# Kernel optimization log

Hardware: AMD Instinct MI355X
Metric: run time of the kernel (lower is better)

The kernel has to match this reference:

```python
import jax, jax.numpy as jnp
import numpy as np

B, L, E = 16, 1022, 1280
D, H, FF, NL = 512, 8, 2048, 4
DH = D // H
EPS = 1e-5


def layer_norm(x, s, b):
    m = jnp.mean(x, axis=-1, keepdims=True)
    v = jnp.mean(jnp.square(x - m), axis=-1, keepdims=True)
    return (x - m) * jax.lax.rsqrt(v + EPS) * s + b


def setup_inputs() -> dict:
    key = jax.random.key(0)
    ks = jax.random.split(key, 12)
    s = 0.02
    return {
        "embeddings": jax.random.normal(ks[0], (B, L, E), jnp.float32),
        "mask": jnp.ones((B, L), jnp.float32),
        "position": jnp.tile(jnp.arange(L, dtype=jnp.int32)[None, :], (B, 1)),
        "proj_w": jax.random.normal(ks[1], (D, E), jnp.float32) * s,
        "proj_b": jnp.zeros((D,), jnp.float32),
        "proj_ln_s": jnp.ones((D,), jnp.float32),
        "proj_ln_b": jnp.zeros((D,), jnp.float32),
        "ln1_s": jnp.ones((NL, D), jnp.float32),
        "ln1_b": jnp.zeros((NL, D), jnp.float32),
        "in_w": jax.random.normal(ks[2], (NL, 3 * D, D), jnp.float32) * s,
        "in_b": jnp.zeros((NL, 3 * D), jnp.float32),
        "out_w": jax.random.normal(ks[3], (NL, D, D), jnp.float32) * s,
        "out_b": jnp.zeros((NL, D), jnp.float32),
        "ln2_s": jnp.ones((NL, D), jnp.float32),
        "ln2_b": jnp.zeros((NL, D), jnp.float32),
        "w1": jax.random.normal(ks[4], (NL, FF, D), jnp.float32) * s,
        "b1": jnp.zeros((NL, FF), jnp.float32),
        "w2": jax.random.normal(ks[5], (NL, D, FF), jnp.float32) * s,
        "b2": jnp.zeros((NL, D), jnp.float32),
        "h1_w": jax.random.normal(ks[6], (128, 2 * D), jnp.float32) * s,
        "h1_b": jnp.zeros((128,), jnp.float32),
        "hln_s": jnp.ones((128,), jnp.float32),
        "hln_b": jnp.zeros((128,), jnp.float32),
        "h2_w": jax.random.normal(ks[7], (1, 128), jnp.float32) * s,
        "h2_b": jnp.zeros((1,), jnp.float32),
    }


def _rope_tables():
    inv_freq = 1.0 / (10000.0 ** (jnp.arange(0, DH, 2, dtype=jnp.float32) / DH))
    t = jnp.arange(L, dtype=jnp.float32)
    freqs = jnp.outer(t, inv_freq)          # [L, DH/2]
    emb = jnp.concatenate([freqs, freqs], axis=-1)  # [L, DH]
    return jnp.cos(emb), jnp.sin(emb)


def _rotate_half(x):
    x1, x2 = jnp.split(x, 2, axis=-1)
    return jnp.concatenate([-x2, x1], axis=-1)


def _apply_rope(x, cos, sin):
    # x: [B, L, D] -> per-head rotation -> [B, L, D]
    xh = x.reshape(B, L, H, DH)
    xh = xh * cos[None, :, None, :] + _rotate_half(xh) * sin[None, :, None, :]
    return xh.reshape(B, L, D)


def _forward(embeddings, mask, proj_w, proj_b, proj_ln_s, proj_ln_b,
             ln1_s, ln1_b, in_w, in_b, out_w, out_b, ln2_s, ln2_b,
             w1, b1, w2, b2, h1_w, h1_b, hln_s, hln_b, h2_w, h2_b):
    cos, sin = _rope_tables()
    x = layer_norm(embeddings @ proj_w.T + proj_b, proj_ln_s, proj_ln_b)  # [B,L,D]
    pad = mask <= 0  # True where padded (~mask.bool())
    scale = 1.0 / jnp.sqrt(jnp.float32(DH))
    for i in range(NL):
        n = layer_norm(x, ln1_s[i], ln1_b[i])
        q_in = _apply_rope(n, cos, sin)
        k_in = _apply_rope(n, cos, sin)
        v_in = n
        wq, wk, wv = jnp.split(in_w[i], 3, axis=0)
        bq, bk, bv = jnp.split(in_b[i], 3, axis=0)
        qh = (q_in @ wq.T + bq).reshape(B, L, H, DH)
        kh = (k_in @ wk.T + bk).reshape(B, L, H, DH)
        vh = (v_in @ wv.T + bv).reshape(B, L, H, DH)
        scores = jnp.einsum('blhd,bmhd->bhlm', qh, kh) * scale
        scores = jnp.where(pad[:, None, None, :], jnp.float32(-1e9), scores)
        attn = jax.nn.softmax(scores, axis=-1)
        o = jnp.einsum('bhlm,bmhd->blhd', attn, vh).reshape(B, L, D)
        x = x + (o @ out_w[i].T + out_b[i])
        n2 = layer_norm(x, ln2_s[i], ln2_b[i])
        x = x + (jax.nn.relu(n2 @ w1[i].T + b1[i]) @ w2[i].T + b2[i])
    # masked mean pool
    gctx = (x * mask[..., None]).sum(axis=1) / mask.sum(axis=1, keepdims=True)  # [B,D]
    combined = jnp.concatenate([x, jnp.broadcast_to(gctx[:, None, :], (B, L, D))], axis=-1)
    h = jax.nn.relu(layer_norm(combined @ h1_w.T + h1_b, hln_s, hln_b))
    logits = (h @ h2_w.T + h2_b).squeeze(-1)  # [B,L]
    return logits


def reference(embeddings, mask, position, proj_w, proj_b, proj_ln_s, proj_ln_b,
              ln1_s, ln1_b, in_w, in_b, out_w, out_b, ln2_s, ln2_b,
              w1, b1, w2, b2, h1_w, h1_b, hln_s, hln_b, h2_w, h2_b):
    # position is accepted for API parity but unused (as in the torch module)
    return _forward(embeddings, mask, proj_w, proj_b, proj_ln_s, proj_ln_b,
                    ln1_s, ln1_b, in_w, in_b, out_w, out_b, ln2_s, ln2_b,
                    w1, b1, w2, b2, h1_w, h1_b, hln_s, hln_b, h2_w, h2_b)
```

## Files before the change

kernel.cpp:

```cpp
#include <hip/hip_runtime.h>
#include <cstdint>
#include <cstddef>

#define B_   16
#define L_   1022
#define E_   1280
#define D_   512
#define H_   8
#define FF_  2048
#define NL_  4
#define DH_  64
#define BL_  (B_*L_)
#define EPS_ 1e-5f

typedef unsigned short u16;
typedef unsigned int   u32;
typedef float f32x4 __attribute__((ext_vector_type(4)));
typedef short s16x8 __attribute__((ext_vector_type(8)));

__device__ __forceinline__ u16 f2bf(float f) {
    u32 u = __builtin_bit_cast(u32, f);
    u += 0x7fffu + ((u >> 16) & 1u);
    return (u16)(u >> 16);
}
__device__ __forceinline__ float bf2f(u16 u) {
    return __builtin_bit_cast(float, (u32)u << 16);
}

__global__ __launch_bounds__(256)
void cast_k(const float* __restrict__ src, u16* __restrict__ dst, int n8) {
    int t = blockIdx.x * 256 + threadIdx.x;
    if (t >= n8) return;
    const float* s = src + (size_t)t * 8;
    float4 a = *(const float4*)(s);
    float4 b = *(const float4*)(s + 4);
    s16x8 o;
    o[0] = (short)f2bf(a.x); o[1] = (short)f2bf(a.y);
    o[2] = (short)f2bf(a.z); o[3] = (short)f2bf(a.w);
    o[4] = (short)f2bf(b.x); o[5] = (short)f2bf(b.y);
    o[6] = (short)f2bf(b.z); o[7] = (short)f2bf(b.w);
    *(s16x8*)(dst + (size_t)t * 8) = o;
}

__global__ __launch_bounds__(256)
void h1cast_k(const float* __restrict__ src, u16* __restrict__ dst) {
    int t = blockIdx.x * 256 + threadIdx.x;
    if (t >= 128 * 512 / 8) return;
    int row = t >> 6, c8 = (t & 63) << 3;
    const float* s = src + (size_t)row * 1024 + c8;
    float4 a = *(const float4*)(s);
    float4 b = *(const float4*)(s + 4);
    s16x8 o;
    o[0] = (short)f2bf(a.x); o[1] = (short)f2bf(a.y);
    o[2] = (short)f2bf(a.z); o[3] = (short)f2bf(a.w);
    o[4] = (short)f2bf(b.x); o[5] = (short)f2bf(b.y);
    o[6] = (short)f2bf(b.z); o[7] = (short)f2bf(b.w);
    *(s16x8*)(dst + (size_t)row * 512 + c8) = o;
}

__global__ void tables_k(float* __restrict__ ct, float* __restrict__ st) {
    int idx = blockIdx.x * blockDim.x + threadIdx.x;
    if (idx >= L_ * DH_) return;
    int l = idx / DH_;
    int d = idx % DH_;
    int j = d & 31;
    float invf = powf(10000.0f, -(float)(2 * j) / (float)DH_);
    float ang = (float)l * invf;
    ct[idx] = cosf(ang);
    st[idx] = sinf(ang);
}

template<bool RELU, bool RESID, bool OUTBF, bool ROWBIAS>
__global__ __launch_bounds__(256)
void mgemm_k(const u16* __restrict__ A, const u16* __restrict__ W,
             const float* __restrict__ bias, const float* __restrict__ resid,
             void* __restrict__ Cout, int M, int N, int K)
{
    constexpr int LDT = 72;
    __shared__ u16 As[128 * LDT];
    __shared__ u16 Ws[128 * LDT];
    const int nt = N >> 7;
    const int bx = blockIdx.x % nt;
    const int by = blockIdx.x / nt;
    const int m0 = by << 7, n0 = bx << 7;
    const int tid = threadIdx.x;
    const int lane = tid & 63, wid = tid >> 6;
    const int wr = wid >> 1, wc = wid & 1;
    const int lr = lane & 15, lk = lane >> 4;

    f32x4 acc[4][4];
#pragma unroll
    for (int m = 0; m < 4; m++)
#pragma unroll
        for (int n = 0; n < 4; n++) acc[m][n] = (f32x4)0.0f;

    for (int k0 = 0; k0 < K; k0 += 64) {
        s16x8 va[4], vw[4];
#pragma unroll
        for (int u = 0; u < 4; u++) {
            int ch = tid + (u << 8);
            int r = ch >> 3, c8 = (ch & 7) << 3;
            int ar = m0 + r; if (ar >= M) ar = M - 1;
            va[u] = *(const s16x8*)(A + (size_t)ar * K + k0 + c8);
            vw[u] = *(const s16x8*)(W + (size_t)(n0 + r) * K + k0 + c8);
        }
        __syncthreads();
#pragma unroll
        for (int u = 0; u < 4; u++) {
            int ch = tid + (u << 8);
            int r = ch >> 3, c8 = (ch & 7) << 3;
            *(s16x8*)&As[r * LDT + c8] = va[u];
            *(s16x8*)&Ws[r * LDT + c8] = vw[u];
        }
        __syncthreads();
#pragma unroll
        for (int kk = 0; kk < 2; kk++) {
            s16x8 af[4], bf[4];
#pragma unroll
            for (int m = 0; m < 4; m++)
                af[m] = *(const s16x8*)&As[(wr * 64 + m * 16 + lr) * LDT + kk * 32 + lk * 8];
#pragma unroll
            for (int n = 0; n < 4; n++)
                bf[n] = *(const s16x8*)&Ws[(wc * 64 + n * 16 + lr) * LDT + kk * 32 + lk * 8];
#pragma unroll
            for (int m = 0; m < 4; m++)
#pragma unroll
                for (int n = 0; n < 4; n++)
                    acc[m][n] = __builtin_amdgcn_mfma_f32_16x16x32_bf16(
                        af[m], bf[n], acc[m][n], 0, 0, 0);
        }
    }

    float bv[4];
    if constexpr (!ROWBIAS) {
#pragma unroll
        for (int n = 0; n < 4; n++) bv[n] = bias[n0 + wc * 64 + n * 16 + lr];
    }
#pragma unroll
    for (int m = 0; m < 4; m++) {
#pragma unroll
        for (int j = 0; j < 4; j++) {
            int row = m0 + wr * 64 + m * 16 + lk * 4 + j;
            if (row >= M) continue;
            const float* rb = nullptr;
            if constexpr (ROWBIAS) rb = bias + (size_t)(row / L_) * N;
#pragma unroll
            for (int n = 0; n < 4; n++) {
                int col = n0 + wc * 64 + n * 16 + lr;
                float c = acc[m][n][j];
                if constexpr (ROWBIAS) c += rb[col];
                else                   c += bv[n];
                if constexpr (RELU) c = fmaxf(c, 0.0f);
                if constexpr (RESID) c += resid[(size_t)row * N + col];
                if constexpr (OUTBF) ((u16*)Cout)[(size_t)row * N + col] = f2bf(c);
                else                 ((float*)Cout)[(size_t)row * N + col] = c;
            }
        }
    }
}

template<int DD, bool RELU, bool OUTBF>
__global__ __launch_bounds__(256)
void ln_k(const float* __restrict__ x, const float* __restrict__ s,
          const float* __restrict__ bb, void* __restrict__ out, int M)
{
    const int lane = threadIdx.x & 63;
    const int row = (blockIdx.x << 2) + (threadIdx.x >> 6);
    if (row >= M) return;
    const float* xr = x + (size_t)row * DD;
    constexpr int NV = DD / 64;
    float v[NV];
    if constexpr (NV == 8) {
        *(float4*)(v)     = *(const float4*)(xr + lane * 8);
        *(float4*)(v + 4) = *(const float4*)(xr + lane * 8 + 4);
    } else {
        float2 t = *(const float2*)(xr + lane * 2);
        v[0] = t.x; v[1] = t.y;
    }
    float sum = 0.f, sq = 0.f;
#pragma unroll
    for (int e = 0; e < NV; e++) { sum += v[e]; sq += v[e] * v[e]; }
#pragma unroll
    for (int msk = 1; msk < 64; msk <<= 1) {
        sum += __shfl_xor(sum, msk);
        sq  += __shfl_xor(sq, msk);
    }
    const float mean = sum * (1.0f / DD);
    const float var  = sq * (1.0f / DD) - mean * mean;
    const float rstd = rsqrtf(var + EPS_);
#pragma unroll
    for (int e = 0; e < NV; e++) {
        int d = lane * NV + e;
        float r = (v[e] - mean) * rstd * s[d] + bb[d];
        if constexpr (RELU) r = fmaxf(r, 0.0f);
        v[e] = r;
    }
    if constexpr (OUTBF) {
        u16* orow = (u16*)out + (size_t)row * DD;
        if constexpr (NV == 8) {
            s16x8 o;
#pragma unroll
            for (int e = 0; e < 8; e++) o[e] = (short)f2bf(v[e]);
            *(s16x8*)(orow + lane * 8) = o;
        } else {
            orow[lane * 2] = f2bf(v[0]); orow[lane * 2 + 1] = f2bf(v[1]);
        }
    } else {
        float* orow = (float*)out + (size_t)row * DD;
        if constexpr (NV == 8) {
            *(float4*)(orow + lane * 8)     = *(float4*)(v);
            *(float4*)(orow + lane * 8 + 4) = *(float4*)(v + 4);
        } else {
            float2 t; t.x = v[0]; t.y = v[1];
            *(float2*)(orow + lane * 2) = t;
        }
    }
}

__global__ __launch_bounds__(256)
void rope_k(const u16* __restrict__ n, const float* __restrict__ ct,
            const float* __restrict__ st, u16* __restrict__ r)
{
    int t = blockIdx.x * 256 + threadIdx.x;
    if (t >= BL_ * D_ / 8) return;
    int idx = t << 3;
    int l = (idx / D_) % L_;
    int d = idx & (D_ - 1);
    int dd = d & 63;
    s16x8 xv = *(const s16x8*)(n + idx);
    int pidx; float sgn;
    if (dd < 32) { pidx = idx + 32; sgn = -1.0f; }
    else         { pidx = idx - 32; sgn =  1.0f; }
    s16x8 pv = *(const s16x8*)(n + pidx);
    float4 c0 = *(const float4*)(ct + l * DH_ + dd);
    float4 c1 = *(const float4*)(ct + l * DH_ + dd + 4);
    float4 s0 = *(const float4*)(st + l * DH_ + dd);
    float4 s1 = *(const float4*)(st + l * DH_ + dd + 4);
    float cc[8] = {c0.x,c0.y,c0.z,c0.w,c1.x,c1.y,c1.z,c1.w};
    float ss[8] = {s0.x,s0.y,s0.z,s0.w,s1.x,s1.y,s1.z,s1.w};
    s16x8 o;
#pragma unroll
    for (int e = 0; e < 8; e++) {
        float xf = bf2f((u16)xv[e]);
        float pf = bf2f((u16)pv[e]);
        o[e] = (short)f2bf(xf * cc[e] + sgn * pf * ss[e]);
    }
    *(s16x8*)(r + idx) = o;
}

__global__ __launch_bounds__(256)
void attn_k(const u16* __restrict__ qk, const u16* __restrict__ v,
            const float* __restrict__ mask, u16* __restrict__ o)
{
    constexpr int LDA = 68;
    __shared__ u16 Kt[64 * LDA];
    __shared__ u16 Vt[64 * LDA];
    __shared__ u16 Pl[64 * LDA];
    const int bh = blockIdx.x >> 3, qt = blockIdx.x & 7;
    const int b = bh >> 3, h = bh & 7;
    const int tid = threadIdx.x;
    const int lane = tid & 63, w = tid >> 6;
    const int lr = lane & 15, lg = lane >> 4;
    const size_t basebl = (size_t)b * L_;

    s16x8 aq[2][2];
#pragma unroll
    for (int g = 0; g < 2; g++) {
        int qrow = qt * 128 + w * 32 + g * 16 + lr;
        int qc = qrow < L_ ? qrow : L_ - 1;
#pragma unroll
        for (int kk = 0; kk < 2; kk++)
            aq[g][kk] = *(const s16x8*)(qk + (basebl + qc) * 1024 + h * DH_ + kk * 32 + lg * 8);
    }

    s16x8 bones;
#pragma unroll
    for (int e = 0; e < 8; e++) bones[e] = (short)0x3F80;

    f32x4 oacc[2][4], ocs[2];
    float m_run[2][4];
#pragma unroll
    for (int g = 0; g < 2; g++) {
        ocs[g] = (f32x4)0.0f;
#pragma unroll
        for (int n = 0; n < 4; n++) oacc[g][n] = (f32x4)0.0f;
#pragma unroll
        for (int j = 0; j < 4; j++) m_run[g][j] = -1e30f;
    }

    const int st_key = tid >> 3;
    const int st_d8 = (tid & 7) << 3;

    for (int kt = 0; kt < 16; kt++) {
        __syncthreads();
#pragma unroll
        for (int u = 0; u < 2; u++) {
            int key = st_key + u * 32;
            int gk = kt * 64 + key; if (gk >= L_) gk = L_ - 1;
            s16x8 kv = *(const s16x8*)(qk + (basebl + gk) * 1024 + 512 + h * DH_ + st_d8);
            s16x8 vv = *(const s16x8*)(v  + (basebl + gk) * D_ + h * DH_ + st_d8);
            *(s16x8*)&Kt[key * LDA + st_d8] = kv;
#pragma unroll
            for (int e = 0; e < 8; e++) Vt[(st_d8 + e) * LDA + key] = (u16)vv[e];
        }
        __syncthreads();

        bool val[4];
#pragma unroll
        for (int n = 0; n < 4; n++) {
            int key = kt * 64 + n * 16 + lr;
            val[n] = (key < L_) && (mask[basebl + key] > 0.0f);
        }

#pragma unroll
        for (int g = 0; g < 2; g++) {
            f32x4 sacc[4];
#pragma unroll
            for (int n = 0; n < 4; n++) {
                sacc[n] = (f32x4)0.0f;
#pragma unroll
                for (int kk = 0; kk < 2; kk++) {
                    s16x8 bk = *(const s16x8*)&Kt[(n * 16 + lr) * LDA + kk * 32 + lg * 8];
                    sacc[n] = __builtin_amdgcn_mfma_f32_16x16x32_bf16(aq[g][kk], bk, sacc[n], 0, 0, 0);
                }
            }
#pragma unroll
            for (int j = 0; j < 4; j++) {
                float sv[4];
#pragma unroll
                for (int n = 0; n < 4; n++)
                    sv[n] = val[n] ? sacc[n][j] * 0.125f : -1e30f;
                float tm = fmaxf(fmaxf(sv[0], sv[1]), fmaxf(sv[2], sv[3]));
#pragma unroll
                for (int msk = 1; msk <= 8; msk <<= 1) tm = fmaxf(tm, __shfl_xor(tm, msk));
                float nm = fmaxf(m_run[g][j], tm);
                float corr = __expf(m_run[g][j] - nm);
                m_run[g][j] = nm;
                ocs[g][j] *= corr;
#pragma unroll
                for (int n = 0; n < 4; n++) {
                    oacc[g][n][j] *= corr;
                    Pl[(w * 16 + lg * 4 + j) * LDA + n * 16 + lr] = f2bf(__expf(sv[n] - nm));
                }
            }
#pragma unroll
            for (int kk = 0; kk < 2; kk++) {
                s16x8 ap = *(const s16x8*)&Pl[(w * 16 + lr) * LDA + kk * 32 + lg * 8];
#pragma unroll
                for (int n = 0; n < 4; n++) {
                    s16x8 bv = *(const s16x8*)&Vt[(n * 16 + lr) * LDA + kk * 32 + lg * 8];
                    oacc[g][n] = __builtin_amdgcn_mfma_f32_16x16x32_bf16(ap, bv, oacc[g][n], 0, 0, 0);
                }
                ocs[g] = __builtin_amdgcn_mfma_f32_16x16x32_bf16(ap, bones, ocs[g], 0, 0, 0);
            }
        }
    }

#pragma unroll
    for (int g = 0; g < 2; g++) {
#pragma unroll
        for (int j = 0; j < 4; j++) {
            int qr = qt * 128 + w * 32 + g * 16 + lg * 4 + j;
            if (qr >= L_) continue;
            float inv = 1.0f / ocs[g][j];
#pragma unroll
            for (int n = 0; n < 4; n++)
                o[(basebl + qr) * D_ + h * DH_ + n * 16 + lr] = f2bf(oacc[g][n][j] * inv);
        }
    }
}

__global__ __launch_bounds__(512)
void pool_k(const float* __restrict__ x, const float* __restrict__ mask,
             float* __restrict__ g)
{
    const int b = blockIdx.x;
    const int d = threadIdx.x;
    float acc = 0.f, ms = 0.f;
    for (int l = 0; l < L_; l++) {
        float mv = mask[b * L_ + l];
        acc += x[((size_t)b * L_ + l) * D_ + d] * mv;
        ms += mv;
    }
    g[b * D_ + d] = acc / ms;
}

__global__ __launch_bounds__(256)
void gpart_k(const float* __restrict__ g, const float* __restrict__ h1w,
             const float* __restrict__ h1b, float* __restrict__ gp)
{
    const int lane = threadIdx.x & 63;
    const int gid = (blockIdx.x << 2) + (threadIdx.x >> 6);
    const int b = gid >> 7, j = gid & 127;
    const float* wr = h1w + (size_t)j * (2 * D_) + D_;
    const float* gr = g + b * D_;
    float4 a0 = *(const float4*)(gr + lane * 8);
    float4 a1 = *(const float4*)(gr + lane * 8 + 4);
    float4 w0 = *(const float4*)(wr + lane * 8);
    float4 w1v = *(const float4*)(wr + lane * 8 + 4);
    float acc = a0.x * w0.x + a0.y * w0.y + a0.z * w0.z + a0.w * w0.w
              + a1.x * w1v.x + a1.y * w1v.y + a1.z * w1v.z + a1.w * w1v.w;
#pragma unroll
    for (int msk = 1; msk < 64; msk <<= 1) acc += __shfl_xor(acc, msk);
    if (lane == 0) gp[b * 128 + j] = acc + h1b[j];
}

__global__ __launch_bounds__(256)
void logits_k(const float* __restrict__ h, const float* __restrict__ w,
              const float* __restrict__ bsc, float* __restrict__ out, int M)
{
    const int lane = threadIdx.x & 63;
    const int row = (blockIdx.x << 2) + (threadIdx.x >> 6);
    if (row >= M) return;
    float2 hv = *(const float2*)(h + (size_t)row * 128 + lane * 2);
    float2 wv = *(const float2*)(w + lane * 2);
    float acc = hv.x * wv.x + hv.y * wv.y;
#pragma unroll
    for (int msk = 1; msk < 64; msk <<= 1) acc += __shfl_xor(acc, msk);
    if (lane == 0) out[row] = acc + bsc[0];
}

extern "C" void kernel_launch(void* const* d_in, const int* in_sizes, int n_in,
                              void* d_out, int out_size, void* d_ws, size_t ws_size,
                              hipStream_t stream)
{
    const float* emb       = (const float*)d_in[0];
    const float* mask      = (const float*)d_in[1];
    const float* proj_w    = (const float*)d_in[3];
    const float* proj_b    = (const float*)d_in[4];
    const float* proj_ln_s = (const float*)d_in[5];
    const float* proj_ln_b = (const float*)d_in[6];
    const float* ln1_s     = (const float*)d_in[7];
    const float* ln1_b     = (const float*)d_in[8];
    const float* in_w      = (const float*)d_in[9];
    const float* in_b      = (const float*)d_in[10];
    const float* out_w     = (const float*)d_in[11];
    const float* out_b     = (const float*)d_in[12];
    const float* ln2_s     = (const float*)d_in[13];
    const float* ln2_b     = (const float*)d_in[14];
    const float* w1        = (const float*)d_in[15];
    const float* b1        = (const float*)d_in[16];
    const float* w2        = (const float*)d_in[17];
    const float* b2        = (const float*)d_in[18];
    const float* h1_w      = (const float*)d_in[19];
    const float* h1_b      = (const float*)d_in[20];
    const float* hln_s     = (const float*)d_in[21];
    const float* hln_b     = (const float*)d_in[22];
    const float* h2_w      = (const float*)d_in[23];
    const float* h2_b      = (const float*)d_in[24];
    float* out = (float*)d_out;

    float* ws = (float*)d_ws;
    const size_t S = (size_t)BL_ * D_;
    float* X  = ws;
    float* Rf = ws + S;
    u16* QKB   = (u16*)(ws + S);
    u16* VB    = (u16*)(ws + 2 * S);
    u16* NbB   = (u16*)(ws + 2 * S) + S;
    u16* FFb16 = (u16*)(ws + 3 * S);
    u16* RopeB = FFb16;
    u16* embB  = FFb16;
    u16* RB    = (u16*)(ws + 4 * S);
    u16* projwB = (u16*)(ws + 5 * S);
    u16* iwB  = projwB + 512 * 1280;
    u16* owB  = iwB + (size_t)NL_ * 3 * D_ * D_;
    u16* w1B  = owB + (size_t)NL_ * D_ * D_;
    u16* w2B  = w1B + (size_t)NL_ * FF_ * D_;
    u16* h1wB = w2B + (size_t)NL_ * D_ * FF_;
    float* CT = ws + 5 * S + 6651904;
    float* ST = CT + L_ * DH_;
    float* GC = ST + L_ * DH_;
    float* GP = GC + B_ * D_;
    float* Hb = Rf;

    const int MT = 128;
    const dim3 blk(256);
    const int lnGrid = (BL_ + 3) / 4;

    cast_k<<<(BL_ * E_ / 8 + 255) / 256, blk, 0, stream>>>(emb, embB, BL_ * E_ / 8);
    cast_k<<<(512 * 1280 / 8 + 255) / 256, blk, 0, stream>>>(proj_w, projwB, 512 * 1280 / 8);
    cast_k<<<(NL_ * 3 * D_ * D_ / 8 + 255) / 256, blk, 0, stream>>>(in_w, iwB, NL_ * 3 * D_ * D_ / 8);
    cast_k<<<(NL_ * D_ * D_ / 8 + 255) / 256, blk, 0, stream>>>(out_w, owB, NL_ * D_ * D_ / 8);
    cast_k<<<(NL_ * FF_ * D_ / 8 + 255) / 256, blk, 0, stream>>>(w1, w1B, NL_ * FF_ * D_ / 8);
    cast_k<<<(NL_ * D_ * FF_ / 8 + 255) / 256, blk, 0, stream>>>(w2, w2B, NL_ * D_ * FF_ / 8);
    h1cast_k<<<(128 * 512 / 8 + 255) / 256, blk, 0, stream>>>(h1_w, h1wB);
    tables_k<<<(L_ * DH_ + 255) / 256, blk, 0, stream>>>(CT, ST);

    mgemm_k<false,false,false,false><<<MT * (D_ / 128), blk, 0, stream>>>(
        embB, projwB, proj_b, nullptr, Rf, BL_, D_, E_);
    ln_k<D_,false,false><<<lnGrid, blk, 0, stream>>>(Rf, proj_ln_s, proj_ln_b, X, BL_);

    for (int i = 0; i < NL_; i++) {
        const u16* iw = iwB + (size_t)i * 3 * D_ * D_;
        const float* ib = in_b + (size_t)i * 3 * D_;
        ln_k<D_,false,true><<<lnGrid, blk, 0, stream>>>(X, ln1_s + i * D_, ln1_b + i * D_, NbB, BL_);
        mgemm_k<false,false,true,false><<<MT * 4, blk, 0, stream>>>(
            NbB, iw + 2 * D_ * D_, ib + 2 * D_, nullptr, VB, BL_, D_, D_);
        rope_k<<<(BL_ * D_ / 8 + 255) / 256, blk, 0, stream>>>(NbB, CT, ST, RopeB);
        mgemm_k<false,false,true,false><<<MT * 8, blk, 0, stream>>>(
            RopeB, iw, ib, nullptr, QKB, BL_, 1024, D_);
        attn_k<<<B_ * H_ * 8, blk, 0, stream>>>(QKB, VB, mask, RB);
        mgemm_k<false,true,false,false><<<MT * 4, blk, 0, stream>>>(
            RB, owB + (size_t)i * D_ * D_, out_b + i * D_, X, X, BL_, D_, D_);
        ln_k<D_,false,true><<<lnGrid, blk, 0, stream>>>(X, ln2_s + i * D_, ln2_b + i * D_, NbB, BL_);
        mgemm_k<true,false,true,false><<<MT * 16, blk, 0, stream>>>(
            NbB, w1B + (size_t)i * FF_ * D_, b1 + i * FF_, nullptr, FFb16, BL_, FF_, D_);
        mgemm_k<false,true,false,false><<<MT * 4, blk, 0, stream>>>(
            FFb16, w2B + (size_t)i * D_ * FF_, b2 + i * D_, X, X, BL_, D_, FF_);
    }

    pool_k<<<B_, dim3(512), 0, stream>>>(X, mask, GC);
    gpart_k<<<(B_ * 128) / 4, blk, 0, stream>>>(GC, h1_w, h1_b, GP);
    cast_k<<<(int)((S / 8 + 255) / 256), blk, 0, stream>>>(X, NbB, (int)(S / 8));
    mgemm_k<false,false,false,true><<<MT * 1, blk, 0, stream>>>(
        NbB, h1wB, GP, nullptr, Hb, BL_, 128, D_);
    ln_k<128,true,false><<<lnGrid, blk, 0, stream>>>(Hb, hln_s, hln_b, Hb, BL_);
    logits_k<<<lnGrid, blk, 0, stream>>>(Hb, h2_w, h2_b, out, BL_);
}
```

Measured before the change: 1.576 ms.

## Restructure attention to keep P in registers and split pooling across blocks

New measurement: 1.468 ms. -6.8%, faster.

```diff
diff --git a/kernel.cpp b/kernel.cpp
--- a/kernel.cpp
+++ b/kernel.cpp
@@ -15,8 +15,10 @@
 
 typedef unsigned short u16;
 typedef unsigned int   u32;
+typedef unsigned long long u64;
 typedef float f32x4 __attribute__((ext_vector_type(4)));
 typedef short s16x8 __attribute__((ext_vector_type(8)));
+typedef u32 u32x4 __attribute__((ext_vector_type(4)));
 
 __device__ __forceinline__ u16 f2bf(float f) {
     u32 u = __builtin_bit_cast(u32, f);
@@ -25,6 +27,9 @@
 }
 __device__ __forceinline__ float bf2f(u16 u) {
     return __builtin_bit_cast(float, (u32)u << 16);
+}
+__device__ __forceinline__ u32 pack2bf(float a, float b) {
+    return (u32)f2bf(a) | ((u32)f2bf(b) << 16);
 }
 
 __global__ __launch_bounds__(256)
@@ -255,41 +260,30 @@
     constexpr int LDA = 68;
     __shared__ u16 Kt[64 * LDA];
     __shared__ u16 Vt[64 * LDA];
-    __shared__ u16 Pl[64 * LDA];
-    const int bh = blockIdx.x >> 3, qt = blockIdx.x & 7;
+    const int bh = blockIdx.x >> 4, qt = blockIdx.x & 15;
     const int b = bh >> 3, h = bh & 7;
     const int tid = threadIdx.x;
     const int lane = tid & 63, w = tid >> 6;
     const int lr = lane & 15, lg = lane >> 4;
     const size_t basebl = (size_t)b * L_;
 
-    s16x8 aq[2][2];
-#pragma unroll
-    for (int g = 0; g < 2; g++) {
-        int qrow = qt * 128 + w * 32 + g * 16 + lr;
-        int qc = qrow < L_ ? qrow : L_ - 1;
-#pragma unroll
-        for (int kk = 0; kk < 2; kk++)
-            aq[g][kk] = *(const s16x8*)(qk + (basebl + qc) * 1024 + h * DH_ + kk * 32 + lg * 8);
-    }
-
-    s16x8 bones;
-#pragma unroll
-    for (int e = 0; e < 8; e++) bones[e] = (short)0x3F80;
-
-    f32x4 oacc[2][4], ocs[2];
-    float m_run[2][4];
-#pragma unroll
-    for (int g = 0; g < 2; g++) {
-        ocs[g] = (f32x4)0.0f;
-#pragma unroll
-        for (int n = 0; n < 4; n++) oacc[g][n] = (f32x4)0.0f;
-#pragma unroll
-        for (int j = 0; j < 4; j++) m_run[g][j] = -1e30f;
-    }
+    const int qrow = qt * 64 + w * 16 + lr;
+    const int qc = qrow < L_ ? qrow : L_ - 1;
+    s16x8 bq[2];
+#pragma unroll
+    for (int kk = 0; kk < 2; kk++)
+        bq[kk] = *(const s16x8*)(qk + (basebl + qc) * 1024 + h * DH_ + kk * 32 + lg * 8);
+
+    f32x4 oacc[4];
+#pragma unroll
+    for (int n = 0; n < 4; n++) oacc[n] = (f32x4)0.0f;
+    float m_run = -1e30f, l_run = 0.f;
 
     const int st_key = tid >> 3;
     const int st_d8 = (tid & 7) << 3;
+    const int src0 = lr + ((lane & 16) << 1);
+    const int src1 = src0 + 16;
+    const bool ahi = (lg >> 1) != 0;
 
     for (int kt = 0; kt < 16; kt++) {
         __syncthreads();
@@ -305,82 +299,128 @@
         }
         __syncthreads();
 
-        bool val[4];
+        int gkey = kt * 64 + lane;
+        bool vb = (gkey < L_) && (mask[basebl + gkey] > 0.0f);
+        u64 vm = __ballot(vb);
+
+        f32x4 sacc[4];
 #pragma unroll
         for (int n = 0; n < 4; n++) {
-            int key = kt * 64 + n * 16 + lr;
-            val[n] = (key < L_) && (mask[basebl + key] > 0.0f);
-        }
-
-#pragma unroll
-        for (int g = 0; g < 2; g++) {
-            f32x4 sacc[4];
-#pragma unroll
-            for (int n = 0; n < 4; n++) {
-                sacc[n] = (f32x4)0.0f;
-#pragma unroll
-                for (int kk = 0; kk < 2; kk++) {
-                    s16x8 bk = *(const s16x8*)&Kt[(n * 16 + lr) * LDA + kk * 32 + lg * 8];
-                    sacc[n] = __builtin_amdgcn_mfma_f32_16x16x32_bf16(aq[g][kk], bk, sacc[n], 0, 0, 0);
-                }
+            sacc[n] = (f32x4)0.0f;
+#pragma unroll
+            for (int kk = 0; kk < 2; kk++) {
+                s16x8 ak = *(const s16x8*)&Kt[(n * 16 + lr) * LDA + kk * 32 + lg * 8];
+                sacc[n] = __builtin_amdgcn_mfma_f32_16x16x32_bf16(ak, bq[kk], sacc[n], 0, 0, 0);
             }
+        }
+
+        float p[4][4];
+        float tm = -1e30f;
+#pragma unroll
+        for (int n = 0; n < 4; n++)
 #pragma unroll
             for (int j = 0; j < 4; j++) {
-                float sv[4];
-#pragma unroll
-                for (int n = 0; n < 4; n++)
-                    sv[n] = val[n] ? sacc[n][j] * 0.125f : -1e30f;
-                float tm = fmaxf(fmaxf(sv[0], sv[1]), fmaxf(sv[2], sv[3]));
-#pragma unroll
-                for (int msk = 1; msk <= 8; msk <<= 1) tm = fmaxf(tm, __shfl_xor(tm, msk));
-                float nm = fmaxf(m_run[g][j], tm);
-                float corr = __expf(m_run[g][j] - nm);
-                m_run[g][j] = nm;
-                ocs[g][j] *= corr;
-#pragma unroll
-                for (int n = 0; n < 4; n++) {
-                    oacc[g][n][j] *= corr;
-                    Pl[(w * 16 + lg * 4 + j) * LDA + n * 16 + lr] = f2bf(__expf(sv[n] - nm));
-                }
+                int kl = 16 * n + 4 * lg + j;
+                float s = ((vm >> kl) & 1ull) ? sacc[n][j] * 0.125f : -1e30f;
+                p[n][j] = s;
+                tm = fmaxf(tm, s);
             }
-#pragma unroll
-            for (int kk = 0; kk < 2; kk++) {
-                s16x8 ap = *(const s16x8*)&Pl[(w * 16 + lr) * LDA + kk * 32 + lg * 8];
-#pragma unroll
-                for (int n = 0; n < 4; n++) {
-                    s16x8 bv = *(const s16x8*)&Vt[(n * 16 + lr) * LDA + kk * 32 + lg * 8];
-                    oacc[g][n] = __builtin_amdgcn_mfma_f32_16x16x32_bf16(ap, bv, oacc[g][n], 0, 0, 0);
-                }
-                ocs[g] = __builtin_amdgcn_mfma_f32_16x16x32_bf16(ap, bones, ocs[g], 0, 0, 0);
+        tm = fmaxf(tm, __shfl_xor(tm, 16));
+        tm = fmaxf(tm, __shfl_xor(tm, 32));
+        float nm = fmaxf(m_run, tm);
+        float corr = __expf(m_run - nm);
+        m_run = nm;
+        float ts = 0.f;
+#pragma unroll
+        for (int n = 0; n < 4; n++)
+#pragma unroll
+            for (int j = 0; j < 4; j++) {
+                p[n][j] = __expf(p[n][j] - nm);
+                ts += p[n][j];
             }
-        }
-    }
-
-#pragma unroll
-    for (int g = 0; g < 2; g++) {
-#pragma unroll
-        for (int j = 0; j < 4; j++) {
-            int qr = qt * 128 + w * 32 + g * 16 + lg * 4 + j;
-            if (qr >= L_) continue;
-            float inv = 1.0f / ocs[g][j];
-#pragma unroll
-            for (int n = 0; n < 4; n++)
-                o[(basebl + qr) * D_ + h * DH_ + n * 16 + lr] = f2bf(oacc[g][n][j] * inv);
-        }
+        ts += __shfl_xor(ts, 16);
+        ts += __shfl_xor(ts, 32);
+        l_run = l_run * corr + ts;
+#pragma unroll
+        for (int n = 0; n < 4; n++) oacc[n] *= corr;
+
+        u32 pk[4][2];
+#pragma unroll
+        for (int n = 0; n < 4; n++) {
+            pk[n][0] = pack2bf(p[n][0], p[n][1]);
+            pk[n][1] = pack2bf(p[n][2], p[n][3]);
+        }
+        u32 r0[4][2], r1[4][2];
+#pragma unroll
+        for (int n = 0; n < 4; n++)
+#pragma unroll
+            for (int i = 0; i < 2; i++) {
+                r0[n][i] = (u32)__shfl((int)pk[n][i], src0);
+                r1[n][i] = (u32)__shfl((int)pk[n][i], src1);
+            }
+#pragma unroll
+        for (int kk = 0; kk < 2; kk++) {
+            u32x4 bw;
+            bw[0] = ahi ? r0[2 * kk + 1][0] : r0[2 * kk][0];
+            bw[1] = ahi ? r0[2 * kk + 1][1] : r0[2 * kk][1];
+            bw[2] = ahi ? r1[2 * kk + 1][0] : r1[2 * kk][0];
+            bw[3] = ahi ? r1[2 * kk + 1][1] : r1[2 * kk][1];
+            s16x8 bp = __builtin_bit_cast(s16x8, bw);
+#pragma unroll
+            for (int n2 = 0; n2 < 4; n2++) {
+                s16x8 av = *(const s16x8*)&Vt[(n2 * 16 + lr) * LDA + kk * 32 + lg * 8];
+                oacc[n2] = __builtin_amdgcn_mfma_f32_16x16x32_bf16(av, bp, oacc[n2], 0, 0, 0);
+            }
+        }
+    }
+
+    __syncthreads();
+    u16* Ol = &Kt[w * 16 * LDA];
+    float inv = 1.0f / l_run;
+#pragma unroll
+    for (int n = 0; n < 4; n++)
+#pragma unroll
+        for (int j = 0; j < 4; j++)
+            Ol[lr * LDA + 16 * n + 4 * lg + j] = f2bf(oacc[n][j] * inv);
+    int orow = lane >> 2, oc = (lane & 3) * 16;
+    int qg = qt * 64 + w * 16 + orow;
+    if (qg < L_) {
+        s16x8 o0 = *(const s16x8*)&Ol[orow * LDA + oc];
+        s16x8 o1 = *(const s16x8*)&Ol[orow * LDA + oc + 8];
+        *(s16x8*)(o + (basebl + qg) * D_ + h * DH_ + oc) = o0;
+        *(s16x8*)(o + (basebl + qg) * D_ + h * DH_ + oc + 8) = o1;
     }
 }
 
 __global__ __launch_bounds__(512)
-void pool_k(const float* __restrict__ x, const float* __restrict__ mask,
+void pool1_k(const float* __restrict__ x, const float* __restrict__ mask,
+             float* __restrict__ pp, float* __restrict__ mp)
+{
+    const int b = blockIdx.x, sp = blockIdx.y;
+    const int d = threadIdx.x;
+    const int l0 = sp * 64;
+    float acc = 0.f;
+    for (int l = l0; l < l0 + 64 && l < L_; l++)
+        acc += x[((size_t)b * L_ + l) * D_ + d] * mask[b * L_ + l];
+    pp[((size_t)b * 16 + sp) * D_ + d] = acc;
+    if (d == 0) {
+        float ms = 0.f;
+        for (int l = l0; l < l0 + 64 && l < L_; l++) ms += mask[b * L_ + l];
+        mp[b * 16 + sp] = ms;
+    }
+}
+
+__global__ __launch_bounds__(512)
+void pool2_k(const float* __restrict__ pp, const float* __restrict__ mp,
              float* __restrict__ g)
 {
     const int b = blockIdx.x;
     const int d = threadIdx.x;
     float acc = 0.f, ms = 0.f;
-    for (int l = 0; l < L_; l++) {
-        float mv = mask[b * L_ + l];
-        acc += x[((size_t)b * L_ + l) * D_ + d] * mv;
-        ms += mv;
+#pragma unroll
+    for (int sp = 0; sp < 16; sp++) {
+        acc += pp[((size_t)b * 16 + sp) * D_ + d];
+        ms += mp[b * 16 + sp];
     }
     g[b * D_ + d] = acc / ms;
 }
@@ -471,6 +511,8 @@
     float* ST = CT + L_ * DH_;
     float* GC = ST + L_ * DH_;
     float* GP = GC + B_ * D_;
+    float* Pp = GP + B_ * 128;
+    float* Mp = Pp + (size_t)B_ * 16 * D_;
     float* Hb = Rf;
 
     const int MT = 128;
@@ -499,7 +541,7 @@
         rope_k<<<(BL_ * D_ / 8 + 255) / 256, blk, 0, stream>>>(NbB, CT, ST, RopeB);
         mgemm_k<false,false,true,false><<<MT * 8, blk, 0, stream>>>(
             RopeB, iw, ib, nullptr, QKB, BL_, 1024, D_);
-        attn_k<<<B_ * H_ * 8, blk, 0, stream>>>(QKB, VB, mask, RB);
+        attn_k<<<B_ * H_ * 16, blk, 0, stream>>>(QKB, VB, mask, RB);
         mgemm_k<false,true,false,false><<<MT * 4, blk, 0, stream>>>(
             RB, owB + (size_t)i * D_ * D_, out_b + i * D_, X, X, BL_, D_, D_);
         ln_k<D_,false,true><<<lnGrid, blk, 0, stream>>>(X, ln2_s + i * D_, ln2_b + i * D_, NbB, BL_);
@@ -509,7 +551,8 @@
             FFb16, w2B + (size_t)i * D_ * FF_, b2 + i * D_, X, X, BL_, D_, FF_);
     }
 
-    pool_k<<<B_, dim3(512), 0, stream>>>(X, mask, GC);
+    pool1_k<<<dim3(B_, 16), dim3(512), 0, stream>>>(X, mask, Pp, Mp);
+    pool2_k<<<B_, dim3(512), 0, stream>>>(Pp, Mp, GC);
     gpart_k<<<(B_ * 128) / 4, blk, 0, stream>>>(GC, h1_w, h1_b, GP);
     cast_k<<<(int)((S / 8 + 255) / 256), blk, 0, stream>>>(X, NbB, (int)(S / 8));
     mgemm_k<false,false,false,true><<<MT * 1, blk, 0, stream>>>(
```
